# Kernel tuning notes

Hardware: AMD Instinct MI355X
Metric: run time of the kernel (lower is better)

The kernel has to match this reference:

```python
import jax, jax.numpy as jnp
import numpy as np

B, L, T = 512, 512, 128


def setup_inputs() -> dict:
    key = jax.random.key(0)
    k0, k1, k2, k3, k4 = jax.random.split(key, 5)
    input_tensors = jax.random.normal(k0, (B, L, T), dtype=jnp.float32)
    # xavier_normal_ for square [T, T]: std = sqrt(2 / (T + T))
    transitions = jax.random.normal(k1, (T, T), dtype=jnp.float32) * np.sqrt(2.0 / (T + T)).astype(np.float32)
    start_transitions = jax.random.normal(k2, (T,), dtype=jnp.float32)
    end_transitions = jax.random.normal(k3, (T,), dtype=jnp.float32)
    label_tensors = jax.random.randint(k4, (B, L), 0, T)
    mask_tensors = jnp.ones((B, L), dtype=jnp.int32)
    return {
        "input_tensors": input_tensors,
        "transitions": transitions,
        "start_transitions": start_transitions,
        "end_transitions": end_transitions,
        "label_tensors": label_tensors,
        "mask_tensors": mask_tensors,
    }


def _crf_nll(input_tensors, transitions, start_transitions, end_transitions,
             label_tensors, mask_tensors):
    maskf = mask_tensors.astype(jnp.float32)  # [B, L]
    # ---------- log-partition (denominator): forward algorithm via scan ----------
    emits = jnp.swapaxes(input_tensors, 0, 1)  # [L, B, T]
    mt = jnp.swapaxes(maskf, 0, 1)             # [L, B]
    alpha0 = start_transitions[None, :] + emits[0]  # [B, T]

    def step(alpha, xs):
        emit_t, m_t = xs  # [B, T], [B]
        # inner[b, i, j] = alpha[b, i] + transitions[i, j] + emit_t[b, j]
        inner = alpha[:, :, None] + transitions[None, :, :] + emit_t[:, None, :]
        new_alpha = jax.nn.logsumexp(inner, axis=1)  # [B, T]
        alpha = new_alpha * m_t[:, None] + alpha * (1.0 - m_t)[:, None]
        return alpha, None

    alpha, _ = jax.lax.scan(step, alpha0, (emits[1:], mt[1:]))
    log_denominator = jax.nn.logsumexp(alpha + end_transitions[None, :], axis=-1)  # [B]

    # ---------- joint (numerator): gold-path score, fully vectorized ----------
    score = start_transitions[label_tensors[:, 0]]  # [B]
    # transition scores between consecutive gold tags, masked by mask[t+1]
    trans_sc = transitions[label_tensors[:, :-1], label_tensors[:, 1:]]  # [B, L-1]
    # emission scores for steps 0..L-2, masked by mask[t]
    emit_sc = jnp.take_along_axis(input_tensors[:, :-1, :], label_tensors[:, :-1, None], axis=2)[..., 0]  # [B, L-1]
    score = score + jnp.sum(trans_sc * maskf[:, 1:] + emit_sc * maskf[:, :-1], axis=1)
    # last valid tag per sequence
    last_idx = maskf.sum(axis=1).astype(jnp.int32) - 1  # [B]
    last_tags = jnp.take_along_axis(label_tensors, last_idx[:, None], axis=1)[:, 0]  # [B]
    last_input_sc = jnp.take_along_axis(input_tensors[:, -1, :], last_tags[:, None], axis=1)[:, 0]  # [B]
    score = score + end_transitions[last_tags] + last_input_sc * maskf[:, -1]

    return jnp.sum(log_denominator - score) / maskf.sum()


def reference(input_tensors, transitions, start_transitions, end_transitions,
              label_tensors, mask_tensors):
    return _crf_nll(input_tensors, transitions, start_transitions, end_transitions,
                    label_tensors, mask_tensors)
```

## Files before the change

kernel.cpp:

```cpp
#include <hip/hip_runtime.h>
#include <hip/hip_bf16.h>

#define Bc 512
#define Lc 512
#define Tc 128
#define GB 16
#define NW 8

typedef __attribute__((ext_vector_type(8))) short bf16x8;
typedef __attribute__((ext_vector_type(4))) float f32x4;
typedef __attribute__((ext_vector_type(2))) unsigned u32x2;

__device__ __forceinline__ void bar_lgkm() {
  asm volatile("s_waitcnt lgkmcnt(0)\n\ts_barrier" ::: "memory");
}
__device__ __forceinline__ unsigned short f2bf_u(float f) {
  __hip_bfloat16 h = __float2bfloat16(f);
  unsigned short us;
  __builtin_memcpy(&us, &h, 2);
  return us;
}
__device__ __forceinline__ short f2bf(float f) { return (short)f2bf_u(f); }
__device__ __forceinline__ unsigned pk2(float a, float b) {
  return (unsigned)f2bf_u(a) | ((unsigned)f2bf_u(b) << 16);
}

__global__ __launch_bounds__(512, 1)
void crf_forward(const float* __restrict__ x,
                 const float* __restrict__ trans,
                 const float* __restrict__ startT,
                 const float* __restrict__ endT,
                 const int*   __restrict__ labels,
                 const int*   __restrict__ mask,
                 float* __restrict__ diff_out,
                 float* __restrict__ msum_out)
{
  __shared__ __align__(16) unsigned short Pl[2][GB * Tc];
  __shared__ __align__(16) float r_s[GB];
  __shared__ unsigned char anyz[Lc];
  __shared__ __align__(16) float c_s[GB];
  __shared__ float score_s[GB];
  __shared__ float msum_s[GB];
  __shared__ float red[GB][NW];

  const int tid  = threadIdx.x;
  const int lane = tid & 63;
  const int w    = tid >> 6;
  const int crow = lane & 15;
  const int khi  = lane >> 4;
  const int bg0  = blockIdx.x * GB;
  const bool rl  = (w == 0) && (khi == 0);

  if (tid < Lc) {
    unsigned zz = 0;
    for (int bb = 0; bb < GB; ++bb)
      zz |= (unsigned)(mask[(size_t)(bg0 + bb) * Lc + tid] == 0);
    anyz[tid] = (unsigned char)zz;
  }

  for (int bb = 2 * w; bb < 2 * w + 2; ++bb) {
    const int bglob = bg0 + bb;
    const int* lbp = labels + (size_t)bglob * Lc;
    const int* mkp = mask + (size_t)bglob * Lc;
    const float* xrow = x + (size_t)bglob * Lc * Tc;
    float sp = 0.f, msp = 0.f;
    for (int t = lane; t < Lc; t += 64) {
      int l0 = lbp[t];
      int m0 = mkp[t];
      msp += (float)m0;
      if (t < Lc - 1) {
        int l1 = lbp[t + 1];
        float m1 = (float)mkp[t + 1];
        sp += trans[l0 * Tc + l1] * m1 + xrow[(size_t)t * Tc + l0] * (float)m0;
      }
    }
#pragma unroll
    for (int off = 32; off; off >>= 1) {
      sp += __shfl_xor(sp, off);
      msp += __shfl_xor(msp, off);
    }
    if (lane == 0) {
      int last_idx = (int)msp - 1;
      int lt = lbp[last_idx];
      score_s[bb] = sp + startT[lbp[0]] + endT[lt]
                  + xrow[(size_t)(Lc - 1) * Tc + lt] * (float)mkp[Lc - 1];
      msum_s[bb] = msp;
    }
  }

  bf16x8 Ef0, Ef1, Ef2, Ef3;
  {
    const int jr = 16 * w + crow;
#pragma unroll
    for (int e = 0; e < 8; ++e) Ef0[e] = f2bf(__expf(trans[(     8 * khi + e) * Tc + jr]));
#pragma unroll
    for (int e = 0; e < 8; ++e) Ef1[e] = f2bf(__expf(trans[(32 + 8 * khi + e) * Tc + jr]));
#pragma unroll
    for (int e = 0; e < 8; ++e) Ef2[e] = f2bf(__expf(trans[(64 + 8 * khi + e) * Tc + jr]));
#pragma unroll
    for (int e = 0; e < 8; ++e) Ef3[e] = f2bf(__expf(trans[(96 + 8 * khi + e) * Tc + jr]));
  }

  const int sw   = (crow & 7) << 3;
  const int boff = crow * Tc;
  const int ro0  = boff + (( 0 + 8 * khi) ^ sw);
  const int ro1  = boff + ((32 + 8 * khi) ^ sw);
  const int ro2  = boff + ((64 + 8 * khi) ^ sw);
  const int ro3  = boff + ((96 + 8 * khi) ^ sw);
  const int wo   = boff + ((16 * w + 4 * khi) ^ sw);
  const float* xp = x + (size_t)(bg0 + crow) * Lc * Tc + 16 * w + 4 * khi;
  const int*   mkl = mask + (size_t)(bg0 + crow) * Lc;

  __syncthreads();

  f32x4 st4 = *(const f32x4*)&startT[16 * w + 4 * khi];
  f32x4 a0  = st4 + *(const f32x4*)xp;
  if (rl) r_s[crow] = a0.x;
  __syncthreads();
  float cb = r_s[crow];
  f32x4 Ao;
  Ao.x = __expf(a0.x - cb); Ao.y = __expf(a0.y - cb);
  Ao.z = __expf(a0.z - cb); Ao.w = __expf(a0.w - cb);
  {
    u32x2 pv = {pk2(Ao.x, Ao.y), pk2(Ao.z, Ao.w)};
    *(u32x2*)&Pl[1][wo] = pv;
  }
  float c  = rl ? cb : 0.f;
  float lr = 0.f;
  __syncthreads();
  if (rl) r_s[crow] = 1.f;
  f32x4 xA = *(const f32x4*)(xp + 1 * Tc);
  f32x4 xB = *(const f32x4*)(xp + 2 * Tc);
  __syncthreads();

#define MFMA_(A, B, C_) C_ = __builtin_amdgcn_mfma_f32_16x16x32_bf16(A, B, C_, 0, 0, 0)
#define STEP(T, RB, WB, PH, XQ) do {                                           \
    bf16x8 Bf0 = *(const bf16x8*)&Pl[RB][ro0];                                 \
    bf16x8 Bf1 = *(const bf16x8*)&Pl[RB][ro1];                                 \
    bf16x8 Bf2 = *(const bf16x8*)&Pl[RB][ro2];                                 \
    bf16x8 Bf3 = *(const bf16x8*)&Pl[RB][ro3];                                 \
    unsigned char az = anyz[T];                                                \
    f32x4 ex;                                                                  \
    ex.x = __expf(XQ.x); ex.y = __expf(XQ.y);                                  \
    ex.z = __expf(XQ.z); ex.w = __expf(XQ.w);                                  \
    { int tp__ = (T) + 2; if (tp__ > Lc - 1) tp__ = Lc - 1;                    \
      XQ = *(const f32x4*)(xp + (size_t)tp__ * Tc); }                          \
    f32x4 Ca = {0.f, 0.f, 0.f, 0.f};                                           \
    f32x4 Cb2 = {0.f, 0.f, 0.f, 0.f};                                          \
    MFMA_(Ef0, Bf0, Ca);  MFMA_(Ef2, Bf2, Cb2);                                \
    MFMA_(Ef1, Bf1, Ca);  MFMA_(Ef3, Bf3, Cb2);                                \
    f32x4 Cr = Ca + Cb2;                                                       \
    f32x4 v;                                                                   \
    if ((PH) == 1) {                                                           \
      float rr = r_s[crow];                                                    \
      v.x = Cr.x * rr * ex.x; v.y = Cr.y * rr * ex.y;                          \
      v.z = Cr.z * rr * ex.z; v.w = Cr.w * rr * ex.w;                          \
    } else {                                                                   \
      v.x = Cr.x * ex.x; v.y = Cr.y * ex.y;                                    \
      v.z = Cr.z * ex.z; v.w = Cr.w * ex.w;                                    \
    }                                                                          \
    if (az) {    \
      int m = mkl[T];                                                          \
      Ao.x = m ? v.x : Ao.x; Ao.y = m ? v.y : Ao.y;                            \
      Ao.z = m ? v.z : Ao.z; Ao.w = m ? v.w : Ao.w;                            \
      if ((PH) == 1 && rl) c += m ? lr : 0.f;                                  \
    } else {                                                                   \
      Ao = v;                                                                  \
      if ((PH) == 1 && rl) c += lr;                                            \
    }                                                                          \
    {                                                                          \
      u32x2 pv = {pk2(Ao.x, Ao.y), pk2(Ao.z, Ao.w)};                           \
      *(u32x2*)&Pl[WB][wo] = pv;                                               \
    }                                                                          \
    if ((PH) == 0 && rl) {            \
      int E0 = (int)((__float_as_uint(Ao.x) >> 23) & 0xffu) - 127;             \
      lr = (float)E0 * 0.6931471805599453f;                                    \
      r_s[crow] = __uint_as_float((unsigned)(127 - E0) << 23);                 \
    }                                                                          \
    bar_lgkm();                                                                \
  } while (0)

  for (int t = 1; t <= Lc - 4; t += 4) {
    STEP(t,     1, 0, 1, xA);
    STEP(t + 1, 0, 1, 2, xB);
    STEP(t + 2, 1, 0, 2, xA);
    STEP(t + 3, 0, 1, 0, xB);
  }
  STEP(Lc - 3, 1, 0, 1, xA);
  STEP(Lc - 2, 0, 1, 2, xB);
  STEP(Lc - 1, 1, 0, 2, xA);
#undef STEP
#undef MFMA_

  if (rl) c_s[crow] = c;
  f32x4 ev = *(const f32x4*)&endT[16 * w + 4 * khi];
  float part = Ao.x * __expf(ev.x) + Ao.y * __expf(ev.y)
             + Ao.z * __expf(ev.z) + Ao.w * __expf(ev.w);
  part += __shfl_xor(part, 16);
  part += __shfl_xor(part, 32);
  if (khi == 0) red[crow][w] = part;
  __syncthreads();
  if (tid < GB) {
    float tot = 0.f;
#pragma unroll
    for (int ww = 0; ww < NW; ++ww) tot += red[tid][ww];
    float logZ = c_s[tid] + __logf(tot);
    diff_out[bg0 + tid] = logZ - score_s[tid];
    msum_out[bg0 + tid] = msum_s[tid];
  }
}

__global__ __launch_bounds__(512)
void crf_final(const float* __restrict__ diff, const float* __restrict__ msum,
               float* __restrict__ out)
{
  __shared__ float sd[512];
  __shared__ float sm[512];
  int t = threadIdx.x;
  sd[t] = diff[t];
  sm[t] = msum[t];
  __syncthreads();
  for (int s = 256; s > 0; s >>= 1) {
    if (t < s) { sd[t] += sd[t + s]; sm[t] += sm[t + s]; }
    __syncthreads();
  }
  if (t == 0) out[0] = sd[0] / sm[0];
}

extern "C" void kernel_launch(void* const* d_in, const int* in_sizes, int n_in,
                              void* d_out, int out_size, void* d_ws, size_t ws_size,
                              hipStream_t stream) {
  const float* x      = (const float*)d_in[0];
  const float* trans  = (const float*)d_in[1];
  const float* startT = (const float*)d_in[2];
  const float* endT   = (const float*)d_in[3];
  const int*   labels = (const int*)d_in[4];
  const int*   mask   = (const int*)d_in[5];
  float* out = (float*)d_out;
  float* ws  = (float*)d_ws;
  float* diff = ws;
  float* msum = ws + Bc;

  crf_forward<<<dim3(Bc / GB), dim3(512), 0, stream>>>(
      x, trans, startT, endT, labels, mask, diff, msum);
  crf_final<<<dim3(1), dim3(512), 0, stream>>>(diff, msum, out);
}
```

Baseline: 171.8 us.

## Halve forward-kernel waves per block, each wave computing two 16-tag output tiles

Result: slower. 214.9 us (+25.1%).

```diff
diff --git a/kernel.cpp b/kernel.cpp
--- a/kernel.cpp
+++ b/kernel.cpp
@@ -5,7 +5,7 @@
 #define Lc 512
 #define Tc 128
 #define GB 16
-#define NW 8
+#define NW 4
 
 typedef __attribute__((ext_vector_type(8))) short bf16x8;
 typedef __attribute__((ext_vector_type(4))) float f32x4;
@@ -25,7 +25,7 @@
   return (unsigned)f2bf_u(a) | ((unsigned)f2bf_u(b) << 16);
 }
 
-__global__ __launch_bounds__(512, 1)
+__global__ __launch_bounds__(256, 1) __attribute__((amdgpu_waves_per_eu(1, 1)))
 void crf_forward(const float* __restrict__ x,
                  const float* __restrict__ trans,
                  const float* __restrict__ startT,
@@ -51,14 +51,14 @@
   const int bg0  = blockIdx.x * GB;
   const bool rl  = (w == 0) && (khi == 0);
 
-  if (tid < Lc) {
+  for (int t = tid; t < Lc; t += 256) {
     unsigned zz = 0;
     for (int bb = 0; bb < GB; ++bb)
-      zz |= (unsigned)(mask[(size_t)(bg0 + bb) * Lc + tid] == 0);
-    anyz[tid] = (unsigned char)zz;
-  }
-
-  for (int bb = 2 * w; bb < 2 * w + 2; ++bb) {
+      zz |= (unsigned)(mask[(size_t)(bg0 + bb) * Lc + t] == 0);
+    anyz[t] = (unsigned char)zz;
+  }
+
+  for (int bb = 4 * w; bb < 4 * w + 4; ++bb) {
     const int bglob = bg0 + bb;
     const int* lbp = labels + (size_t)bglob * Lc;
     const int* mkp = mask + (size_t)bglob * Lc;
@@ -88,17 +88,21 @@
     }
   }
 
-  bf16x8 Ef0, Ef1, Ef2, Ef3;
+  bf16x8 E00, E01, E02, E03, E10, E11, E12, E13;
   {
-    const int jr = 16 * w + crow;
+    const int jr0 = 32 * w + crow;
+    const int jr1 = jr0 + 16;
 #pragma unroll
-    for (int e = 0; e < 8; ++e) Ef0[e] = f2bf(__expf(trans[(     8 * khi + e) * Tc + jr]));
-#pragma unroll
-    for (int e = 0; e < 8; ++e) Ef1[e] = f2bf(__expf(trans[(32 + 8 * khi + e) * Tc + jr]));
-#pragma unroll
-    for (int e = 0; e < 8; ++e) Ef2[e] = f2bf(__expf(trans[(64 + 8 * khi + e) * Tc + jr]));
-#pragma unroll
-    for (int e = 0; e < 8; ++e) Ef3[e] = f2bf(__expf(trans[(96 + 8 * khi + e) * Tc + jr]));
+    for (int e = 0; e < 8; ++e) {
+      E00[e] = f2bf(__expf(trans[(     8 * khi + e) * Tc + jr0]));
+      E01[e] = f2bf(__expf(trans[(32 + 8 * khi + e) * Tc + jr0]));
+      E02[e] = f2bf(__expf(trans[(64 + 8 * khi + e) * Tc + jr0]));
+      E03[e] = f2bf(__expf(trans[(96 + 8 * khi + e) * Tc + jr0]));
+      E10[e] = f2bf(__expf(trans[(     8 * khi + e) * Tc + jr1]));
+      E11[e] = f2bf(__expf(trans[(32 + 8 * khi + e) * Tc + jr1]));
+      E12[e] = f2bf(__expf(trans[(64 + 8 * khi + e) * Tc + jr1]));
+      E13[e] = f2bf(__expf(trans[(96 + 8 * khi + e) * Tc + jr1]));
+    }
   }
 
   const int sw   = (crow & 7) << 3;
@@ -107,95 +111,120 @@
   const int ro1  = boff + ((32 + 8 * khi) ^ sw);
   const int ro2  = boff + ((64 + 8 * khi) ^ sw);
   const int ro3  = boff + ((96 + 8 * khi) ^ sw);
-  const int wo   = boff + ((16 * w + 4 * khi) ^ sw);
-  const float* xp = x + (size_t)(bg0 + crow) * Lc * Tc + 16 * w + 4 * khi;
+  const int wo0  = boff + ((32 * w      + 4 * khi) ^ sw);
+  const int wo1  = boff + ((32 * w + 16 + 4 * khi) ^ sw);
+  const float* xp = x + (size_t)(bg0 + crow) * Lc * Tc + 32 * w + 4 * khi;
   const int*   mkl = mask + (size_t)(bg0 + crow) * Lc;
 
   __syncthreads();
 
-  f32x4 st4 = *(const f32x4*)&startT[16 * w + 4 * khi];
-  f32x4 a0  = st4 + *(const f32x4*)xp;
-  if (rl) r_s[crow] = a0.x;
+  f32x4 st0 = *(const f32x4*)&startT[32 * w + 4 * khi];
+  f32x4 st1 = *(const f32x4*)&startT[32 * w + 16 + 4 * khi];
+  f32x4 a00 = st0 + *(const f32x4*)xp;
+  f32x4 a01 = st1 + *(const f32x4*)(xp + 16);
+  if (rl) r_s[crow] = a00.x;
   __syncthreads();
   float cb = r_s[crow];
-  f32x4 Ao;
-  Ao.x = __expf(a0.x - cb); Ao.y = __expf(a0.y - cb);
-  Ao.z = __expf(a0.z - cb); Ao.w = __expf(a0.w - cb);
+  f32x4 Ao0, Ao1;
+  Ao0.x = __expf(a00.x - cb); Ao0.y = __expf(a00.y - cb);
+  Ao0.z = __expf(a00.z - cb); Ao0.w = __expf(a00.w - cb);
+  Ao1.x = __expf(a01.x - cb); Ao1.y = __expf(a01.y - cb);
+  Ao1.z = __expf(a01.z - cb); Ao1.w = __expf(a01.w - cb);
   {
-    u32x2 pv = {pk2(Ao.x, Ao.y), pk2(Ao.z, Ao.w)};
-    *(u32x2*)&Pl[1][wo] = pv;
+    u32x2 p0 = {pk2(Ao0.x, Ao0.y), pk2(Ao0.z, Ao0.w)};
+    u32x2 p1 = {pk2(Ao1.x, Ao1.y), pk2(Ao1.z, Ao1.w)};
+    *(u32x2*)&Pl[1][wo0] = p0;
+    *(u32x2*)&Pl[1][wo1] = p1;
   }
   float c  = rl ? cb : 0.f;
   float lr = 0.f;
   __syncthreads();
   if (rl) r_s[crow] = 1.f;
-  f32x4 xA = *(const f32x4*)(xp + 1 * Tc);
-  f32x4 xB = *(const f32x4*)(xp + 2 * Tc);
+  f32x4 xA0 = *(const f32x4*)(xp + 1 * Tc);
+  f32x4 xA1 = *(const f32x4*)(xp + 1 * Tc + 16);
+  f32x4 xB0 = *(const f32x4*)(xp + 2 * Tc);
+  f32x4 xB1 = *(const f32x4*)(xp + 2 * Tc + 16);
   __syncthreads();
 
 #define MFMA_(A, B, C_) C_ = __builtin_amdgcn_mfma_f32_16x16x32_bf16(A, B, C_, 0, 0, 0)
-#define STEP(T, RB, WB, PH, XQ) do {                                           \
+#define STEP(T, RB, WB, PH, XQ0, XQ1) do {                                     \
     bf16x8 Bf0 = *(const bf16x8*)&Pl[RB][ro0];                                 \
     bf16x8 Bf1 = *(const bf16x8*)&Pl[RB][ro1];                                 \
     bf16x8 Bf2 = *(const bf16x8*)&Pl[RB][ro2];                                 \
     bf16x8 Bf3 = *(const bf16x8*)&Pl[RB][ro3];                                 \
     unsigned char az = anyz[T];                                                \
-    f32x4 ex;                                                                  \
-    ex.x = __expf(XQ.x); ex.y = __expf(XQ.y);                                  \
-    ex.z = __expf(XQ.z); ex.w = __expf(XQ.w);                                  \
+    f32x4 ex0, ex1;                                                            \
+    ex0.x = __expf(XQ0.x); ex0.y = __expf(XQ0.y);                              \
+    ex0.z = __expf(XQ0.z); ex0.w = __expf(XQ0.w);                              \
+    ex1.x = __expf(XQ1.x); ex1.y = __expf(XQ1.y);                              \
+    ex1.z = __expf(XQ1.z); ex1.w = __expf(XQ1.w);                              \
     { int tp__ = (T) + 2; if (tp__ > Lc - 1) tp__ = Lc - 1;                    \
-      XQ = *(const f32x4*)(xp + (size_t)tp__ * Tc); }                          \
-    f32x4 Ca = {0.f, 0.f, 0.f, 0.f};                                           \
-    f32x4 Cb2 = {0.f, 0.f, 0.f, 0.f};                                          \
-    MFMA_(Ef0, Bf0, Ca);  MFMA_(Ef2, Bf2, Cb2);                                \
-    MFMA_(Ef1, Bf1, Ca);  MFMA_(Ef3, Bf3, Cb2);                                \
-    f32x4 Cr = Ca + Cb2;                                                       \
-    f32x4 v;                                                                   \
+      XQ0 = *(const f32x4*)(xp + (size_t)tp__ * Tc);                           \
+      XQ1 = *(const f32x4*)(xp + (size_t)tp__ * Tc + 16); }                    \
+    f32x4 Ca0 = {0.f,0.f,0.f,0.f}, Cb0 = {0.f,0.f,0.f,0.f};                    \
+    f32x4 Ca1 = {0.f,0.f,0.f,0.f}, Cb1 = {0.f,0.f,0.f,0.f};                    \
+    MFMA_(E00, Bf0, Ca0); MFMA_(E10, Bf0, Ca1);                                \
+    MFMA_(E02, Bf2, Cb0); MFMA_(E12, Bf2, Cb1);                                \
+    MFMA_(E01, Bf1, Ca0); MFMA_(E11, Bf1, Ca1);                                \
+    MFMA_(E03, Bf3, Cb0); MFMA_(E13, Bf3, Cb1);                                \
+    f32x4 Cr0 = Ca0 + Cb0, Cr1 = Ca1 + Cb1;                                    \
+    f32x4 v0, v1;                                                              \
     if ((PH) == 1) {                                                           \
       float rr = r_s[crow];                                                    \
-      v.x = Cr.x * rr * ex.x; v.y = Cr.y * rr * ex.y;                          \
-      v.z = Cr.z * rr * ex.z; v.w = Cr.w * rr * ex.w;                          \
+      v0.x = Cr0.x * rr * ex0.x; v0.y = Cr0.y * rr * ex0.y;                    \
+      v0.z = Cr0.z * rr * ex0.z; v0.w = Cr0.w * rr * ex0.w;                    \
+      v1.x = Cr1.x * rr * ex1.x; v1.y = Cr1.y * rr * ex1.y;                    \
+      v1.z = Cr1.z * rr * ex1.z; v1.w = Cr1.w * rr * ex1.w;                    \
     } else {                                                                   \
-      v.x = Cr.x * ex.x; v.y = Cr.y * ex.y;                                    \
-      v.z = Cr.z * ex.z; v.w = Cr.w * ex.w;                                    \
-    }                                                                          \
-    if (az) {    \
+      v0.x = Cr0.x * ex0.x; v0.y = Cr0.y * ex0.y;                              \
+      v0.z = Cr0.z * ex0.z; v0.w = Cr0.w * ex0.w;                              \
+      v1.x = Cr1.x * ex1.x; v1.y = Cr1.y * ex1.y;                              \
+      v1.z = Cr1.z * ex1.z; v1.w = Cr1.w * ex1.w;                              \
+    }                                                                          \
+    if (az) {                     \
       int m = mkl[T];                                                          \
-      Ao.x = m ? v.x : Ao.x; Ao.y = m ? v.y : Ao.y;                            \
-      Ao.z = m ? v.z : Ao.z; Ao.w = m ? v.w : Ao.w;                            \
+      Ao0.x = m ? v0.x : Ao0.x; Ao0.y = m ? v0.y : Ao0.y;                      \
+      Ao0.z = m ? v0.z : Ao0.z; Ao0.w = m ? v0.w : Ao0.w;                      \
+      Ao1.x = m ? v1.x : Ao1.x; Ao1.y = m ? v1.y : Ao1.y;                      \
+      Ao1.z = m ? v1.z : Ao1.z; Ao1.w = m ? v1.w : Ao1.w;                      \
       if ((PH) == 1 && rl) c += m ? lr : 0.f;                                  \
     } else {                                                                   \
-      Ao = v;                                                                  \
+      Ao0 = v0; Ao1 = v1;                                                      \
       if ((PH) == 1 && rl) c += lr;                                            \
     }                                                                          \
     {                                                                          \
-      u32x2 pv = {pk2(Ao.x, Ao.y), pk2(Ao.z, Ao.w)};                           \
-      *(u32x2*)&Pl[WB][wo] = pv;                                               \
+      u32x2 p0 = {pk2(Ao0.x, Ao0.y), pk2(Ao0.z, Ao0.w)};                       \
+      u32x2 p1 = {pk2(Ao1.x, Ao1.y), pk2(Ao1.z, Ao1.w)};                       \
+      *(u32x2*)&Pl[WB][wo0] = p0;                                              \
+      *(u32x2*)&Pl[WB][wo1] = p1;                                              \
     }                                                                          \
     if ((PH) == 0 && rl) {            \
-      int E0 = (int)((__float_as_uint(Ao.x) >> 23) & 0xffu) - 127;             \
-      lr = (float)E0 * 0.6931471805599453f;                                    \
-      r_s[crow] = __uint_as_float((unsigned)(127 - E0) << 23);                 \
+      int E_ = (int)((__float_as_uint(Ao0.x) >> 23) & 0xffu) - 127;            \
+      lr = (float)E_ * 0.6931471805599453f;                                    \
+      r_s[crow] = __uint_as_float((unsigned)(127 - E_) << 23);                 \
     }                                                                          \
     bar_lgkm();                                                                \
   } while (0)
 
   for (int t = 1; t <= Lc - 4; t += 4) {
-    STEP(t,     1, 0, 1, xA);
-    STEP(t + 1, 0, 1, 2, xB);
-    STEP(t + 2, 1, 0, 2, xA);
-    STEP(t + 3, 0, 1, 0, xB);
-  }
-  STEP(Lc - 3, 1, 0, 1, xA);
-  STEP(Lc - 2, 0, 1, 2, xB);
-  STEP(Lc - 1, 1, 0, 2, xA);
+    STEP(t,     1, 0, 1, xA0, xA1);
+    STEP(t + 1, 0, 1, 2, xB0, xB1);
+    STEP(t + 2, 1, 0, 2, xA0, xA1);
+    STEP(t + 3, 0, 1, 0, xB0, xB1);
+  }
+  STEP(Lc - 3, 1, 0, 1, xA0, xA1);
+  STEP(Lc - 2, 0, 1, 2, xB0, xB1);
+  STEP(Lc - 1, 1, 0, 2, xA0, xA1);
 #undef STEP
 #undef MFMA_
 
   if (rl) c_s[crow] = c;
-  f32x4 ev = *(const f32x4*)&endT[16 * w + 4 * khi];
-  float part = Ao.x * __expf(ev.x) + Ao.y * __expf(ev.y)
-             + Ao.z * __expf(ev.z) + Ao.w * __expf(ev.w);
+  f32x4 ev0 = *(const f32x4*)&endT[32 * w + 4 * khi];
+  f32x4 ev1 = *(const f32x4*)&endT[32 * w + 16 + 4 * khi];
+  float part = Ao0.x * __expf(ev0.x) + Ao0.y * __expf(ev0.y)
+             + Ao0.z * __expf(ev0.z) + Ao0.w * __expf(ev0.w)
+             + Ao1.x * __expf(ev1.x) + Ao1.y * __expf(ev1.y)
+             + Ao1.z * __expf(ev1.z) + Ao1.w * __expf(ev1.w);
   part += __shfl_xor(part, 16);
   part += __shfl_xor(part, 32);
   if (khi == 0) red[crow][w] = part;
@@ -241,7 +270,7 @@
   float* diff = ws;
   float* msum = ws + Bc;
 
-  crf_forward<<<dim3(Bc / GB), dim3(512), 0, stream>>>(
+  crf_forward<<<dim3(Bc / GB), dim3(256), 0, stream>>>(
       x, trans, startT, endT, labels, mask, diff, msum);
   crf_final<<<dim3(1), dim3(512), 0, stream>>>(diff, msum, out);
 }
```
